# Kernel optimization log

Measured on AMD Instinct MI355X. Metric: run time of the kernel, lower is better.

The kernel has to match this reference:

```python
import jax, jax.numpy as jnp
import numpy as np

HEADS = 16


def setup_inputs() -> dict:
    key = jax.random.key(0)
    ks = jax.random.split(key, 6)
    b, n, c = 4, 2048, 1024  # batch, seq_len, query_dim (== hidden_dim)
    h = 1024                 # hidden_dim = heads * dim_head = 16 * 64
    s = 0.02
    return {
        "x": jax.random.normal(ks[0], (b, n, c), jnp.float32),
        "Wq": jax.random.normal(ks[1], (h, c), jnp.float32) * s,
        "Wk": jax.random.normal(ks[2], (h, c), jnp.float32) * s,
        "Wv": jax.random.normal(ks[3], (h, c), jnp.float32) * s,
        "Wout": jax.random.normal(ks[4], (c, h), jnp.float32) * s,
        "bout": jnp.zeros((c,), jnp.float32),
    }


def reference(x, Wq, Wk, Wv, Wout, bout):
    # x: (b, n, c). Self-attention (context = x).
    b, n, c = x.shape
    m = HEADS
    d = Wq.shape[0] // m  # dim_head
    # 1x1 conv == linear projection over channel dim
    q = jnp.einsum('bnc,hc->bnh', x, Wq).reshape(b, n, m, d)
    k = jnp.einsum('bnc,hc->bnh', x, Wk).reshape(b, n, m, d)
    v = jnp.einsum('bnc,hc->bnh', x, Wv).reshape(b, n, m, d)
    scale = d ** (-0.25)  # 1/sqrt(sqrt(d)), applied to both q and k
    # weight: (b, m, n_q, n_k)
    weight = jnp.einsum('bimd,bjmd->bmij', q * scale, k * scale)
    weight = jax.nn.softmax(weight, axis=-1)
    a = jnp.einsum('bmij,bjmd->bimd', weight, v).reshape(b, n, m * d)
    return jnp.einsum('bnh,ch->bnc', a, Wout) + bout
```

## Files before the change

### kernel.cpp

```cpp
#include <hip/hip_runtime.h>
#include <stdint.h>
#include <stddef.h>

typedef __attribute__((ext_vector_type(4))) float f32x4;
typedef __attribute__((ext_vector_type(16))) float f32x16;
typedef __attribute__((ext_vector_type(8))) short s16x8;
typedef __attribute__((ext_vector_type(4))) short s16x4;

__device__ __forceinline__ short f2bf(float f) {
  uint32_t u = __builtin_bit_cast(uint32_t, f);
  uint32_t r = (u + 0x7fffu + ((u >> 16) & 1u)) >> 16;
  return (short)r;
}

__device__ __forceinline__ void gload_lds16(const void* g, void* l) {
  __builtin_amdgcn_global_load_lds(
      (const __attribute__((address_space(1))) void*)g,
      (__attribute__((address_space(3))) void*)l, 16, 0, 0);
}

__device__ __forceinline__ int msk8(int r) { return (r & 7) ^ ((r >> 3) & 7); }
__device__ __forceinline__ int swz(int r, int c) {
  return r * 64 + (c ^ (msk8(r) << 3));
}
__device__ __forceinline__ int swv(int d) { return d ^ ((d >> 3) & 3); }

__global__ __launch_bounds__(256) void cvt_kernel(const float* __restrict__ src,
                                                  short* __restrict__ dst, int n4) {
  int i = blockIdx.x * blockDim.x + threadIdx.x;
  if (i >= n4) return;
  float4 v = reinterpret_cast<const float4*>(src)[i];
  s16x4 o;
  o[0] = f2bf(v.x); o[1] = f2bf(v.y); o[2] = f2bf(v.z); o[3] = f2bf(v.w);
  reinterpret_cast<s16x4*>(dst)[i] = o;
}

__global__ __launch_bounds__(256) void cvt_w(const float* __restrict__ Wq,
                                             const float* __restrict__ Wk,
                                             const float* __restrict__ Wv,
                                             const float* __restrict__ Wout,
                                             short* __restrict__ Wqkv,
                                             short* __restrict__ Woutb) {
  int i = blockIdx.x * 256 + threadIdx.x;
  int g = i >> 18, li = i & 262143;
  const float* src = g == 0 ? Wq : g == 1 ? Wk : g == 2 ? Wv : Wout;
  short* dst = g < 3 ? Wqkv + (size_t)g * 1048576 : Woutb;
  float4 v = reinterpret_cast<const float4*>(src)[li];
  s16x4 o;
  o[0] = f2bf(v.x); o[1] = f2bf(v.y); o[2] = f2bf(v.z); o[3] = f2bf(v.w);
  reinterpret_cast<s16x4*>(dst)[li] = o;
}

template <int OUTF32>
__global__ __launch_bounds__(256) void gemm_bt(const short* __restrict__ A,
                                               const short* __restrict__ B,
                                               void* __restrict__ Cv,
                                               const float* __restrict__ bias,
                                               int M, int N, int K,
                                               float qscl, int qcols) {
  __shared__ short lA[128 * 64];
  __shared__ short lB[128 * 64];
  const int tid = threadIdx.x;
  const int lane = tid & 63, wid = tid >> 6;
  const int g = lane >> 4, li = lane & 15;
  const int nbx = N >> 7;
  const int q8 = gridDim.x >> 3;
  const int orig = blockIdx.x;
  const int bswz = (orig & 7) * q8 + (orig >> 3);
  const int by = bswz / nbx, bx = bswz % nbx;
  const int brow = by << 7, bcol = bx << 7;
  const int wr = (wid >> 1) << 6, wc = (wid & 1) << 6;

  f32x4 acc[4][4] = {};

  for (int k0 = 0; k0 < K; k0 += 64) {
    __syncthreads();
#pragma unroll
    for (int i = 0; i < 4; i++) {
      int j = tid + i * 256;
      int r = j >> 3, s = j & 7;
      gload_lds16(A + (size_t)(brow + r) * K + k0 + 8 * (s ^ msk8(r)), &lA[j * 8]);
    }
#pragma unroll
    for (int i = 0; i < 4; i++) {
      int j = tid + i * 256;
      int r = j >> 3, s = j & 7;
      gload_lds16(B + (size_t)(bcol + r) * K + k0 + 8 * (s ^ msk8(r)), &lB[j * 8]);
    }
    __syncthreads();
#pragma unroll
    for (int ks = 0; ks < 2; ks++) {
      s16x8 af[4], bfr[4];
#pragma unroll
      for (int ai = 0; ai < 4; ai++) {
        int row = wr + ai * 16 + li;
        af[ai] = *(const s16x8*)&lA[swz(row, ks * 32 + g * 8)];
      }
#pragma unroll
      for (int bj = 0; bj < 4; bj++) {
        int row = wc + bj * 16 + li;
        bfr[bj] = *(const s16x8*)&lB[swz(row, ks * 32 + g * 8)];
      }
#pragma unroll
      for (int ai = 0; ai < 4; ai++)
#pragma unroll
        for (int bj = 0; bj < 4; bj++)
          acc[ai][bj] = __builtin_amdgcn_mfma_f32_16x16x32_bf16(af[ai], bfr[bj],
                                                               acc[ai][bj], 0, 0, 0);
    }
  }

#pragma unroll
  for (int ai = 0; ai < 4; ai++) {
#pragma unroll
    for (int bj = 0; bj < 4; bj++) {
#pragma unroll
      for (int e = 0; e < 4; e++) {
        int row = brow + wr + ai * 16 + g * 4 + e;
        int col = bcol + wc + bj * 16 + li;
        float v = acc[ai][bj][e];
        if (col < qcols) v *= qscl;
        if (OUTF32) {
          ((float*)Cv)[(size_t)row * N + col] = v + bias[col];
        } else {
          ((short*)Cv)[(size_t)row * N + col] = f2bf(v);
        }
      }
    }
  }
}

__global__ __launch_bounds__(256, 4) void attn_kernel(const short* __restrict__ qkv,
                                                      short* __restrict__ aout) {
  __shared__ short lds[2][8192];

  const int tid = threadIdx.x;
  const int lane = tid & 63, w = tid >> 6;
  const int l31 = lane & 31, hi = lane >> 5;
  const int bid = blockIdx.x;
  const int qt = bid & 15, head = (bid >> 4) & 15, b = bid >> 8;
  const int row0 = b * 2048;
  const int qrow = qt * 128 + w * 32 + l31;
  const int qcol = head * 64, kcol = 1024 + head * 64, vcol = 2048 + head * 64;

#pragma unroll
  for (int s = 0; s < 4; s++)
    gload_lds16(qkv + (size_t)(row0 + qrow) * 3072 + qcol + 16 * s + 8 * hi,
                &lds[0][(w * 4 + s) * 512]);
  __syncthreads();
  s16x8 qf[4];
#pragma unroll
  for (int s = 0; s < 4; s++)
    qf[s] = *(const s16x8*)&lds[0][(w * 4 + s) * 512 + lane * 8];
  __syncthreads();

  const int vj = tid >> 3, va = tid & 7;
  const int vks = vj >> 4;
  const int vphi = (vj >> 2) & 1;
  const int veV = (vj & 3) + 4 * ((vj >> 3) & 1);
  const int vdd = va >> 2, va3 = va & 7 & 3;
  const int vbase = (vks * 2 + vdd) * 512 + vphi * 256 + va3 * 64 + veV;
  const int vslot_r = (32 * hi + swv(l31)) * 8;

#pragma unroll
  for (int sub = 0; sub < 2; sub++)
    gload_lds16(qkv + (size_t)(row0 + sub * 32 + l31) * 3072 + kcol + 16 * w + 8 * hi,
                &lds[0][(sub * 4 + w) * 512]);
#pragma unroll
  for (int sub = 0; sub < 2; sub++) {
    s16x8 v0 = *(const s16x8*)(qkv + (size_t)(row0 + sub * 32 + vj) * 3072 + vcol + 8 * va);
#pragma unroll
    for (int t2 = 0; t2 < 8; t2++)
      lds[0][4096 + sub * 2048 + vbase + 8 * (t2 ^ va3)] = v0[t2];
  }
  __syncthreads();

  f32x16 acc0 = {}, acc1 = {};
  float m2 = -1e30f, l_r = 0.f;
  const float THR = 8.f * 1.44269504088896f;

  for (int jt = 0; jt < 32; jt++) {
    const int cur = jt & 1, nxt = cur ^ 1;
    const int jnext = (jt + 1) * 64;
    const bool pf = (jt < 31);

    s16x8 vs0, vs1;
    if (pf) {
      vs0 = *(const s16x8*)(qkv + (size_t)(row0 + jnext + vj) * 3072 + vcol + 8 * va);
      vs1 = *(const s16x8*)(qkv + (size_t)(row0 + jnext + 32 + vj) * 3072 + vcol + 8 * va);
#pragma unroll
      for (int sub = 0; sub < 2; sub++)
        gload_lds16(qkv + (size_t)(row0 + jnext + sub * 32 + l31) * 3072 + kcol +
                        16 * w + 8 * hi,
                    &lds[nxt][(sub * 4 + w) * 512]);
    }

    f32x16 st0 = {}, st1 = {};
    const short* lc = &lds[cur][0];
    __builtin_amdgcn_s_setprio(1);
#pragma unroll
    for (int s = 0; s < 4; s++) {
      s16x8 kf0 = *(const s16x8*)&lc[s * 512 + lane * 8];
      s16x8 kf1 = *(const s16x8*)&lc[(4 + s) * 512 + lane * 8];
      st0 = __builtin_amdgcn_mfma_f32_32x32x16_bf16(kf0, qf[s], st0, 0, 0, 0);
      st1 = __builtin_amdgcn_mfma_f32_32x32x16_bf16(kf1, qf[s], st1, 0, 0, 0);
    }
    __builtin_amdgcn_s_setprio(0);

    f32x16 mx;
#pragma unroll
    for (int r = 0; r < 16; r++) mx[r] = fmaxf(st0[r], st1[r]);
    float pm = fmaxf(mx[0], mx[1]);
#pragma unroll
    for (int r = 2; r < 16; r += 2) pm = fmaxf(fmaxf(pm, mx[r]), mx[r + 1]);
    pm = fmaxf(pm, __shfl_xor(pm, 32, 64));
    if (__any(pm > m2 + THR)) {
      float mn = fmaxf(m2, pm);
      float al = exp2f(m2 - mn);
      m2 = mn;
      l_r *= al;
      acc0 *= al;
      acc1 *= al;
    }
    st0 = st0 - m2;
    st1 = st1 - m2;
#pragma unroll
    for (int r = 0; r < 16; r++) st0[r] = exp2f(st0[r]);
#pragma unroll
    for (int r = 0; r < 16; r++) st1[r] = exp2f(st1[r]);
    f32x16 sm = st0 + st1;
    float rs = 0.f;
#pragma unroll
    for (int r = 0; r < 8; r++) sm[r] = sm[r] + sm[r + 8];
#pragma unroll
    for (int r = 0; r < 4; r++) sm[r] = sm[r] + sm[r + 4];
    rs = (sm[0] + sm[1]) + (sm[2] + sm[3]);
    rs += __shfl_xor(rs, 32, 64);
    l_r += rs;

    if (pf) {
      short* dst = &lds[nxt][4096];
#pragma unroll
      for (int t2 = 0; t2 < 8; t2++) {
        int off = vbase + 8 * (t2 ^ va3);
        dst[off] = vs0[t2];
        dst[2048 + off] = vs1[t2];
      }
    }

    const short* lV = &lds[cur][4096];
    __builtin_amdgcn_s_setprio(1);
#pragma unroll
    for (int sub = 0; sub < 2; sub++) {
      const f32x16& pp = sub ? st1 : st0;
#pragma unroll
      for (int ks = 0; ks < 2; ks++) {
        int w0, w1, w2, w3;
        asm("v_cvt_pk_bf16_f32 %0, %1, %2" : "=v"(w0) : "v"(pp[8*ks+0]), "v"(pp[8*ks+1]));
        asm("v_cvt_pk_bf16_f32 %0, %1, %2" : "=v"(w1) : "v"(pp[8*ks+2]), "v"(pp[8*ks+3]));
        asm("v_cvt_pk_bf16_f32 %0, %1, %2" : "=v"(w2) : "v"(pp[8*ks+4]), "v"(pp[8*ks+5]));
        asm("v_cvt_pk_bf16_f32 %0, %1, %2" : "=v"(w3) : "v"(pp[8*ks+6]), "v"(pp[8*ks+7]));
        int4 paw;
        paw.x = w0; paw.y = w1; paw.z = w2; paw.w = w3;
        s16x8 pa = __builtin_bit_cast(s16x8, paw);
        s16x8 v0 = *(const s16x8*)&lV[sub * 2048 + (ks * 2 + 0) * 512 + vslot_r];
        s16x8 v1 = *(const s16x8*)&lV[sub * 2048 + (ks * 2 + 1) * 512 + vslot_r];
        acc0 = __builtin_amdgcn_mfma_f32_32x32x16_bf16(v0, pa, acc0, 0, 0, 0);
        acc1 = __builtin_amdgcn_mfma_f32_32x32x16_bf16(v1, pa, acc1, 0, 0, 0);
      }
    }
    __builtin_amdgcn_s_setprio(0);

    __syncthreads();
  }

  float inv = 1.f / l_r;
  const size_t rowoff = (size_t)(row0 + qt * 128 + w * 32 + l31) * 1024 + head * 64;
#pragma unroll
  for (int rq = 0; rq < 4; rq++) {
    s16x4 o0, o1;
#pragma unroll
    for (int i2 = 0; i2 < 4; i2++) {
      o0[i2] = f2bf(acc0[rq * 4 + i2] * inv);
      o1[i2] = f2bf(acc1[rq * 4 + i2] * inv);
    }
    int dbase = 8 * rq + 4 * hi;
    *(s16x4*)&aout[rowoff + dbase] = o0;
    *(s16x4*)&aout[rowoff + 32 + dbase] = o1;
  }
}

extern "C" void kernel_launch(void* const* d_in, const int* in_sizes, int n_in,
                              void* d_out, int out_size, void* d_ws, size_t ws_size,
                              hipStream_t stream) {
  const float* x    = (const float*)d_in[0];
  const float* Wq   = (const float*)d_in[1];
  const float* Wk   = (const float*)d_in[2];
  const float* Wv   = (const float*)d_in[3];
  const float* Wout = (const float*)d_in[4];
  const float* bout = (const float*)d_in[5];
  float* out = (float*)d_out;

  char* ws = (char*)d_ws;
  short* xb    = (short*)(ws);
  short* Wqkv  = (short*)(ws + (16ull << 20));
  short* Woutb = (short*)(ws + (22ull << 20));
  short* qkv   = (short*)(ws + (24ull << 20));
  short* a_ws  = xb;

  const float SCL = 0.125f * 1.44269504088896f;

  cvt_kernel<<<8192, 256, 0, stream>>>(x, xb, 2097152);
  cvt_w<<<4096, 256, 0, stream>>>(Wq, Wk, Wv, Wout, Wqkv, Woutb);

  gemm_bt<0><<<64 * 24, 256, 0, stream>>>(xb, Wqkv, qkv, nullptr, 8192, 3072, 1024,
                                          SCL, 1024);

  attn_kernel<<<1024, 256, 0, stream>>>(qkv, a_ws);

  gemm_bt<1><<<64 * 8, 256, 0, stream>>>(a_ws, Woutb, out, bout, 8192, 1024, 1024,
                                         1.f, 0);
}
```

Baseline: 303.5 us.

## Use 64-row tiles for output GEMM and fold max subtraction into QK accumulator init

The output projection moves to a new 64x128-tile GEMM kernel launched with 1024 blocks instead of 512, so more blocks can fill the compute units on this smaller GEMM. The attention kernel drops the per-tile subtraction of the running max. It seeds the QK MFMA accumulators with a negated running-max vector and subtracts only when the threshold is exceeded, which saves VALU work on the common path. The max reduction is also reorganised into a shallower tree. The cost is smaller tiles with less reuse per load in the output GEMM, plus a subtle change to how the softmax max is tracked.

```diff
diff --git a/kernel.cpp b/kernel.cpp
--- a/kernel.cpp
+++ b/kernel.cpp
@@ -51,11 +51,9 @@
   reinterpret_cast<s16x4*>(dst)[li] = o;
 }
 
-template <int OUTF32>
 __global__ __launch_bounds__(256) void gemm_bt(const short* __restrict__ A,
                                                const short* __restrict__ B,
-                                               void* __restrict__ Cv,
-                                               const float* __restrict__ bias,
+                                               short* __restrict__ Cb,
                                                int M, int N, int K,
                                                float qscl, int qcols) {
   __shared__ short lA[128 * 64];
@@ -120,11 +118,78 @@
         int col = bcol + wc + bj * 16 + li;
         float v = acc[ai][bj][e];
         if (col < qcols) v *= qscl;
-        if (OUTF32) {
-          ((float*)Cv)[(size_t)row * N + col] = v + bias[col];
-        } else {
-          ((short*)Cv)[(size_t)row * N + col] = f2bf(v);
-        }
+        Cb[(size_t)row * N + col] = f2bf(v);
+      }
+    }
+  }
+}
+
+__global__ __launch_bounds__(256) void gemm_bt64(const short* __restrict__ A,
+                                                 const short* __restrict__ B,
+                                                 float* __restrict__ C,
+                                                 const float* __restrict__ bias,
+                                                 int M, int N, int K) {
+  __shared__ short lA[64 * 64];
+  __shared__ short lB[128 * 64];
+  const int tid = threadIdx.x;
+  const int lane = tid & 63, wid = tid >> 6;
+  const int g = lane >> 4, li = lane & 15;
+  const int nbx = N >> 7;
+  const int q8 = gridDim.x >> 3;
+  const int orig = blockIdx.x;
+  const int bswz = (orig & 7) * q8 + (orig >> 3);
+  const int by = bswz / nbx, bx = bswz % nbx;
+  const int brow = by << 6, bcol = bx << 7;
+  const int wr = (wid >> 1) << 5, wc = (wid & 1) << 6;
+
+  f32x4 acc[2][4] = {};
+
+  for (int k0 = 0; k0 < K; k0 += 64) {
+    __syncthreads();
+#pragma unroll
+    for (int i = 0; i < 2; i++) {
+      int j = tid + i * 256;
+      int r = j >> 3, s = j & 7;
+      gload_lds16(A + (size_t)(brow + r) * K + k0 + 8 * (s ^ msk8(r)), &lA[j * 8]);
+    }
+#pragma unroll
+    for (int i = 0; i < 4; i++) {
+      int j = tid + i * 256;
+      int r = j >> 3, s = j & 7;
+      gload_lds16(B + (size_t)(bcol + r) * K + k0 + 8 * (s ^ msk8(r)), &lB[j * 8]);
+    }
+    __syncthreads();
+#pragma unroll
+    for (int ks = 0; ks < 2; ks++) {
+      s16x8 af[2], bfr[4];
+#pragma unroll
+      for (int ai = 0; ai < 2; ai++) {
+        int row = wr + ai * 16 + li;
+        af[ai] = *(const s16x8*)&lA[swz(row, ks * 32 + g * 8)];
+      }
+#pragma unroll
+      for (int bj = 0; bj < 4; bj++) {
+        int row = wc + bj * 16 + li;
+        bfr[bj] = *(const s16x8*)&lB[swz(row, ks * 32 + g * 8)];
+      }
+#pragma unroll
+      for (int ai = 0; ai < 2; ai++)
+#pragma unroll
+        for (int bj = 0; bj < 4; bj++)
+          acc[ai][bj] = __builtin_amdgcn_mfma_f32_16x16x32_bf16(af[ai], bfr[bj],
+                                                               acc[ai][bj], 0, 0, 0);
+    }
+  }
+
+#pragma unroll
+  for (int ai = 0; ai < 2; ai++) {
+#pragma unroll
+    for (int bj = 0; bj < 4; bj++) {
+#pragma unroll
+      for (int e = 0; e < 4; e++) {
+        int row = brow + wr + ai * 16 + g * 4 + e;
+        int col = bcol + wc + bj * 16 + li;
+        C[(size_t)row * N + col] = acc[ai][bj][e] + bias[col];
       }
     }
   }
@@ -158,7 +223,7 @@
   const int vks = vj >> 4;
   const int vphi = (vj >> 2) & 1;
   const int veV = (vj & 3) + 4 * ((vj >> 3) & 1);
-  const int vdd = va >> 2, va3 = va & 7 & 3;
+  const int vdd = va >> 2, va3 = va & 3;
   const int vbase = (vks * 2 + vdd) * 512 + vphi * 256 + va3 * 64 + veV;
   const int vslot_r = (32 * hi + swv(l31)) * 8;
 
@@ -176,7 +241,8 @@
   __syncthreads();
 
   f32x16 acc0 = {}, acc1 = {};
-  float m2 = -1e30f, l_r = 0.f;
+  f32x16 nm = {};
+  float l_r = 0.f;
   const float THR = 8.f * 1.44269504088896f;
 
   for (int jt = 0; jt < 32; jt++) {
@@ -195,7 +261,7 @@
                     &lds[nxt][(sub * 4 + w) * 512]);
     }
 
-    f32x16 st0 = {}, st1 = {};
+    f32x16 st0 = nm, st1 = nm;
     const short* lc = &lds[cur][0];
     __builtin_amdgcn_s_setprio(1);
 #pragma unroll
@@ -210,31 +276,33 @@
     f32x16 mx;
 #pragma unroll
     for (int r = 0; r < 16; r++) mx[r] = fmaxf(st0[r], st1[r]);
-    float pm = fmaxf(mx[0], mx[1]);
-#pragma unroll
-    for (int r = 2; r < 16; r += 2) pm = fmaxf(fmaxf(pm, mx[r]), mx[r + 1]);
+    float a0 = fmaxf(fmaxf(mx[0], mx[1]), mx[2]);
+    float a1 = fmaxf(fmaxf(mx[3], mx[4]), mx[5]);
+    float a2 = fmaxf(fmaxf(mx[6], mx[7]), mx[8]);
+    float a3 = fmaxf(fmaxf(mx[9], mx[10]), mx[11]);
+    float a4 = fmaxf(fmaxf(mx[12], mx[13]), mx[14]);
+    float pm = fmaxf(fmaxf(fmaxf(a0, a1), fmaxf(a2, a3)), fmaxf(a4, mx[15]));
     pm = fmaxf(pm, __shfl_xor(pm, 32, 64));
-    if (__any(pm > m2 + THR)) {
-      float mn = fmaxf(m2, pm);
-      float al = exp2f(m2 - mn);
-      m2 = mn;
+    if (__any(pm > THR)) {
+      float d = fmaxf(pm, 0.f);
+      float al = exp2f(-d);
       l_r *= al;
       acc0 *= al;
       acc1 *= al;
-    }
-    st0 = st0 - m2;
-    st1 = st1 - m2;
+      nm -= d;
+      st0 -= d;
+      st1 -= d;
+    }
 #pragma unroll
     for (int r = 0; r < 16; r++) st0[r] = exp2f(st0[r]);
 #pragma unroll
     for (int r = 0; r < 16; r++) st1[r] = exp2f(st1[r]);
     f32x16 sm = st0 + st1;
-    float rs = 0.f;
 #pragma unroll
     for (int r = 0; r < 8; r++) sm[r] = sm[r] + sm[r + 8];
 #pragma unroll
     for (int r = 0; r < 4; r++) sm[r] = sm[r] + sm[r + 4];
-    rs = (sm[0] + sm[1]) + (sm[2] + sm[3]);
+    float rs = (sm[0] + sm[1]) + (sm[2] + sm[3]);
     rs += __shfl_xor(rs, 32, 64);
     l_r += rs;
 
@@ -313,11 +381,9 @@
   cvt_kernel<<<8192, 256, 0, stream>>>(x, xb, 2097152);
   cvt_w<<<4096, 256, 0, stream>>>(Wq, Wk, Wv, Wout, Wqkv, Woutb);
 
-  gemm_bt<0><<<64 * 24, 256, 0, stream>>>(xb, Wqkv, qkv, nullptr, 8192, 3072, 1024,
-                                          SCL, 1024);
+  gemm_bt<<<64 * 24, 256, 0, stream>>>(xb, Wqkv, qkv, 8192, 3072, 1024, SCL, 1024);
 
   attn_kernel<<<1024, 256, 0, stream>>>(qkv, a_ws);
 
-  gemm_bt<1><<<64 * 8, 256, 0, stream>>>(a_ws, Woutb, out, bout, 8192, 1024, 1024,
-                                         1.f, 0);
-}
+  gemm_bt64<<<1024, 256, 0, stream>>>(a_ws, Woutb, out, bout, 8192, 1024, 1024);
+}
```

Measured after the change: 322.3 us. +6.2%, slower.
